# Kernel tuning notes

Hardware: AMD Instinct MI355X
Metric: run time of the kernel (lower is better)

The kernel has to match this reference:

```python
import jax, jax.numpy as jnp
import numpy as np

jax.config.update("jax_enable_x64", True)  # original module runs the filter in float64

SR = 24000
N_CHANNELS = 64
F_MIN, F_MAX = 10.0, 100.0
R_MIN, R_MAX = 0.9999, 0.99999
BATCH, T = 8, 24000


def _make_coeffs():
    # Mirrors BidirectionalCursedIIR.__init__ buffer construction
    freqs = np.exp(np.linspace(np.log(F_MIN), np.log(F_MAX), N_CHANNELS))
    radii = np.linspace(R_MIN, R_MAX, N_CHANNELS)
    theta = 2.0 * np.pi * freqs / SR
    a0 = np.ones_like(radii)
    a1 = -2.0 * radii * np.cos(theta)
    a2 = radii ** 2
    b0 = (1.0 - radii) * 0.5
    a = np.stack([a0, a1, a2], axis=1)                      # [C, 3]
    b = np.stack([b0, np.zeros_like(b0), np.zeros_like(b0)], axis=1)  # [C, 3]
    return jnp.asarray(a, jnp.float64), jnp.asarray(b, jnp.float64)


def _iir_bank(x2d, a1, a2, b0):
    # x2d: [B, T] float64; per-channel recurrence y[n] = b0*x[n] - a1*y[n-1] - a2*y[n-2]
    B = x2d.shape[0]
    C = a1.shape[0]
    z = jnp.zeros((B, C), x2d.dtype)

    def step(carry, xt):  # xt: [B]
        y1, y2 = carry
        y = b0[None, :] * xt[:, None] - a1[None, :] * y1 - a2[None, :] * y2
        return (y, y1), y

    _, ys = jax.lax.scan(step, (z, z), jnp.moveaxis(x2d, 1, 0))  # ys: [T, B, C]
    return jnp.transpose(ys, (1, 2, 0))  # [B, C, T]


def setup_inputs() -> dict:
    key = jax.random.key(0)
    x = jax.random.normal(key, (BATCH, 1, T), dtype=jnp.float32)
    a_coeffs, b_coeffs = _make_coeffs()
    return {"x": x, "a_coeffs": a_coeffs, "b_coeffs": b_coeffs}


def reference(x, a_coeffs, b_coeffs):
    # a0 == 1 by construction, so the normalization by a0 is a no-op
    a1, a2 = a_coeffs[:, 1], a_coeffs[:, 2]
    b0 = b_coeffs[:, 0]
    xd = x[:, 0, :].astype(jnp.float64)  # [B, T]
    fwd_state = _iir_bank(xd, a1, a2, b0)                 # forward pass
    bwd_state = _iir_bank(xd[:, ::-1], a1, a2, b0)[:, :, ::-1]  # flipped pass
    return jnp.concatenate([fwd_state, bwd_state], axis=1).astype(jnp.float32)  # [B, 2C, T]
```

## Files before the change

kernel.cpp:

```cpp
#include <hip/hip_runtime.h>
#include <math.h>

#define T_LEN 24000
#define NCH   64
#define NSEQ  16
#define LCH   192
#define KCH   125
#define KGRP  25

static_assert(KCH * LCH == T_LEN, "chunking must cover T");
static_assert(KCH % KGRP == 0, "grouping must cover KCH");

#define CF_DBL   448
#define ST_DBL   ((size_t)NSEQ * NCH * KCH * 2)
#define WS_FAST  ((CF_DBL + 2 * ST_DBL) * sizeof(double))
#define WS_MID   ((CF_DBL + ST_DBL) * sizeof(double))

__global__ __launch_bounds__(64) void iir_coeffs(double* __restrict__ cf) {
    const int c = threadIdx.x;
    const double l10 = log(10.0), l100 = log(100.0);
    double lf = (c == 63) ? l100 : l10 + (double)c * ((l100 - l10) / 63.0);
    double f  = exp(lf);
    double r  = (c == 63) ? 0.99999
                          : 0.9999 + (double)c * ((0.99999 - 0.9999) / 63.0);
    double th = (2.0 * M_PI) * f / 24000.0;
    double a1 = (-2.0 * r) * cos(th), a2 = r * r, b0 = (1.0 - r) * 0.5;
    double pj1 = 1.0, pj2 = 0.0, pj3 = 0.0;
    #pragma unroll 16
    for (int j = 0; j < LCH; ++j) {
        double p = fma(-a1, pj1, -a2 * pj2);
        pj3 = pj2; pj2 = pj1; pj1 = p;
    }
    cf[0 * 64 + c] = a1;
    cf[1 * 64 + c] = a2;
    cf[2 * 64 + c] = b0;
    cf[3 * 64 + c] = pj1;
    cf[4 * 64 + c] = -a2 * pj2;
    cf[5 * 64 + c] = pj2;
    cf[6 * 64 + c] = -a2 * pj3;
}

__global__ __launch_bounds__(64) void iir_phase1(
        const float* __restrict__ x, const double* __restrict__ cf,
        double* __restrict__ stEnd) {
    __shared__ float xs[LCH];
    const int g = blockIdx.x, k = g % KCH, s = g / KCH;
    const int bi = s >> 1, dir = s & 1, c = threadIdx.x;
    const double a1 = cf[c], a2 = cf[64 + c], b0 = cf[128 + c];
    const float* xb = x + (size_t)bi * T_LEN;
    const int t0 = k * LCH;
    #pragma unroll
    for (int w = 0; w < LCH / 64; ++w) {
        const int t = t0 + w * 64 + c;
        xs[w * 64 + c] = (dir == 0) ? xb[t] : xb[T_LEN - 1 - t];
    }
    __syncthreads();
    double y1 = 0.0, y2 = 0.0;
    #pragma unroll 16
    for (int j = 0; j < LCH; ++j) {
        double y = fma(-a1, y1, fma(-a2, y2, b0 * (double)xs[j]));
        y2 = y1; y1 = y;
    }
    ((double2*)stEnd)[((size_t)k * NSEQ + s) * NCH + c] = make_double2(y1, y2);
}

__global__ __launch_bounds__(64) void iir_phase2(
        const double* __restrict__ cf, const double* __restrict__ stEnd,
        double* __restrict__ stEntry) {
    __shared__ double2 ls[KGRP * NCH];
    const int s = blockIdx.x, c = threadIdx.x;
    const double A00 = cf[192 + c], A01 = cf[256 + c];
    const double A10 = cf[320 + c], A11 = cf[384 + c];
    const double2* src = (const double2*)stEnd;
    double2* dst = (double2*)stEntry;
    double in1 = 0.0, in2 = 0.0;
    for (int g = 0; g < KCH / KGRP; ++g) {
        const int kb = g * KGRP;
        #pragma unroll
        for (int j = 0; j < KGRP; ++j)
            ls[j * NCH + c] = src[((size_t)(kb + j) * NSEQ + s) * NCH + c];
        __syncthreads();
        #pragma unroll
        for (int j = 0; j < KGRP; ++j) {
            const double2 e = ls[j * NCH + c];
            dst[((size_t)(kb + j) * NSEQ + s) * NCH + c] =
                make_double2(in1, in2);
            const double n1 = e.x + fma(A00, in1, A01 * in2);
            const double n2 = e.y + fma(A10, in1, A11 * in2);
            in1 = n1; in2 = n2;
        }
        __syncthreads();
    }
}

__global__ __launch_bounds__(64) void iir_phase2_inplace(
        const double* __restrict__ cf, double* st) {
    __shared__ double2 ls[KGRP * NCH];
    const int s = blockIdx.x, c = threadIdx.x;
    const double A00 = cf[192 + c], A01 = cf[256 + c];
    const double A10 = cf[320 + c], A11 = cf[384 + c];
    double2* buf = (double2*)st;
    double in1 = 0.0, in2 = 0.0;
    for (int g = 0; g < KCH / KGRP; ++g) {
        const int kb = g * KGRP;
        for (int j = 0; j < KGRP; ++j)
            ls[j * NCH + c] = buf[((size_t)(kb + j) * NSEQ + s) * NCH + c];
        __syncthreads();
        for (int j = 0; j < KGRP; ++j) {
            const double2 e = ls[j * NCH + c];
            buf[((size_t)(kb + j) * NSEQ + s) * NCH + c] =
                make_double2(in1, in2);
            const double n1 = e.x + fma(A00, in1, A01 * in2);
            const double n2 = e.y + fma(A10, in1, A11 * in2);
            in1 = n1; in2 = n2;
        }
        __syncthreads();
    }
}

__global__ __launch_bounds__(64) void iir_phase3(
        const float* __restrict__ x, const double* __restrict__ cf,
        const double* __restrict__ stEntry, float* __restrict__ out) {
    __shared__ float xs[LCH];
    __shared__ float tile[NCH][65];
    const int g = blockIdx.x, k = g % KCH, s = g / KCH;
    const int bi = s >> 1, dir = s & 1, c = threadIdx.x;
    const double a1 = cf[c], a2 = cf[64 + c], b0 = cf[128 + c];
    const double2 ent = ((const double2*)stEntry)[((size_t)k * NSEQ + s) * NCH + c];
    double y1 = ent.x, y2 = ent.y;
    const float* xb = x + (size_t)bi * T_LEN;
    const int t0 = k * LCH;
    #pragma unroll
    for (int w = 0; w < LCH / 64; ++w) {
        const int t = t0 + w * 64 + c;
        xs[w * 64 + c] = (dir == 0) ? xb[t] : xb[T_LEN - 1 - t];
    }
    __syncthreads();
    for (int w = 0; w < LCH / 64; ++w) {
        #pragma unroll 16
        for (int jw = 0; jw < 64; ++jw) {
            double y = fma(-a1, y1, fma(-a2, y2, b0 * (double)xs[w * 64 + jw]));
            y2 = y1; y1 = y;
            tile[c][jw] = (float)y;
        }
        __syncthreads();
        const int tw0 = t0 + w * 64;
        if (dir == 0) {
            #pragma unroll
            for (int r = 0; r < NCH; ++r)
                out[((size_t)(bi * 128 + r)) * T_LEN + (tw0 + c)] = tile[r][c];
        } else {
            #pragma unroll
            for (int r = 0; r < NCH; ++r)
                out[((size_t)(bi * 128 + 64 + r)) * T_LEN +
                    (T_LEN - 1 - (tw0 + c))] = tile[r][c];
        }
        __syncthreads();
    }
}

__device__ __forceinline__ void channel_coeffs_dev(int c, double& a1,
                                                   double& a2, double& b0) {
    const double l10 = log(10.0), l100 = log(100.0);
    double lf = (c == 63) ? l100 : l10 + (double)c * ((l100 - l10) / 63.0);
    double f = exp(lf);
    double r = (c == 63) ? 0.99999
                         : 0.9999 + (double)c * ((0.99999 - 0.9999) / 63.0);
    double th = (2.0 * M_PI) * f / 24000.0;
    a1 = (-2.0 * r) * cos(th); a2 = r * r; b0 = (1.0 - r) * 0.5;
}

__global__ __launch_bounds__(64) void iir_direct(
        const float* __restrict__ x, float* __restrict__ out) {
    __shared__ float tile[NCH][65];
    const int s = blockIdx.x, bi = s >> 1, dir = s & 1, c = threadIdx.x;
    double a1, a2, b0;
    channel_coeffs_dev(c, a1, a2, b0);
    const float* xb = x + (size_t)bi * T_LEN;
    double y1 = 0.0, y2 = 0.0;
    for (int t0 = 0; t0 < T_LEN; t0 += 64) {
        #pragma unroll 8
        for (int j = 0; j < 64; ++j) {
            const int t = t0 + j;
            double xv = (dir == 0) ? (double)xb[t] : (double)xb[T_LEN - 1 - t];
            double y = fma(-a1, y1, fma(-a2, y2, b0 * xv));
            y2 = y1; y1 = y;
            tile[c][j] = (float)y;
        }
        __syncthreads();
        if (dir == 0) {
            #pragma unroll
            for (int r = 0; r < NCH; ++r)
                out[((size_t)(bi * 128 + r)) * T_LEN + (t0 + c)] = tile[r][c];
        } else {
            #pragma unroll
            for (int r = 0; r < NCH; ++r)
                out[((size_t)(bi * 128 + 64 + r)) * T_LEN +
                    (T_LEN - 1 - (t0 + c))] = tile[r][c];
        }
        __syncthreads();
    }
}

extern "C" void kernel_launch(void* const* d_in, const int* in_sizes, int n_in,
                              void* d_out, int out_size, void* d_ws, size_t ws_size,
                              hipStream_t stream) {
    const float* x = (const float*)d_in[0];
    float* out = (float*)d_out;
    double* ws = (double*)d_ws;

    if (d_ws != nullptr && ws_size >= WS_FAST) {
        double* cf = ws;
        double* stEnd = ws + CF_DBL;
        double* stEntry = ws + CF_DBL + ST_DBL;
        iir_coeffs<<<1, 64, 0, stream>>>(cf);
        iir_phase1<<<NSEQ * KCH, 64, 0, stream>>>(x, cf, stEnd);
        iir_phase2<<<NSEQ, 64, 0, stream>>>(cf, stEnd, stEntry);
        iir_phase3<<<NSEQ * KCH, 64, 0, stream>>>(x, cf, stEntry, out);
    } else if (d_ws != nullptr && ws_size >= WS_MID) {
        double* cf = ws;
        double* st = ws + CF_DBL;
        iir_coeffs<<<1, 64, 0, stream>>>(cf);
        iir_phase1<<<NSEQ * KCH, 64, 0, stream>>>(x, cf, st);
        iir_phase2_inplace<<<NSEQ, 64, 0, stream>>>(cf, st);
        iir_phase3<<<NSEQ * KCH, 64, 0, stream>>>(x, cf, st, out);
    } else {
        iir_direct<<<NSEQ, 64, 0, stream>>>(x, out);
    }
}
```

Measured before the change: 42.30 us.

## Fold coefficient and carry-propagation kernels into endstate and output kernels

Replaces the four-launch pipeline (coeffs, phase1, serial phase2 scan, phase3) with two launches. Each endstate block computes its channel coefficients inline, and block 0 also writes the chunk-transition matrix. Each output block then redoes the cross-chunk carry scan itself by reading all preceding chunk end states, so the serial 16-block phase2 kernel and the extra launches go away. The cost is redundant O(k) dependent loads and FMAs per block, up to 124 steps for the last chunks, which lengthens the critical path of late blocks.

```diff
diff --git a/kernel.cpp b/kernel.cpp
--- a/kernel.cpp
+++ b/kernel.cpp
@@ -6,47 +6,34 @@
 #define NSEQ  16
 #define LCH   192
 #define KCH   125
-#define KGRP  25
 
 static_assert(KCH * LCH == T_LEN, "chunking must cover T");
-static_assert(KCH % KGRP == 0, "grouping must cover KCH");
 
 #define CF_DBL   448
 #define ST_DBL   ((size_t)NSEQ * NCH * KCH * 2)
-#define WS_FAST  ((CF_DBL + 2 * ST_DBL) * sizeof(double))
-#define WS_MID   ((CF_DBL + ST_DBL) * sizeof(double))
+#define WS_NEED  ((CF_DBL + ST_DBL) * sizeof(double))
 
-__global__ __launch_bounds__(64) void iir_coeffs(double* __restrict__ cf) {
-    const int c = threadIdx.x;
+__device__ __forceinline__ void channel_coeffs_dev(int c, double& a1,
+                                                   double& a2, double& b0) {
     const double l10 = log(10.0), l100 = log(100.0);
     double lf = (c == 63) ? l100 : l10 + (double)c * ((l100 - l10) / 63.0);
     double f  = exp(lf);
     double r  = (c == 63) ? 0.99999
                           : 0.9999 + (double)c * ((0.99999 - 0.9999) / 63.0);
     double th = (2.0 * M_PI) * f / 24000.0;
-    double a1 = (-2.0 * r) * cos(th), a2 = r * r, b0 = (1.0 - r) * 0.5;
-    double pj1 = 1.0, pj2 = 0.0, pj3 = 0.0;
-    #pragma unroll 16
-    for (int j = 0; j < LCH; ++j) {
-        double p = fma(-a1, pj1, -a2 * pj2);
-        pj3 = pj2; pj2 = pj1; pj1 = p;
-    }
-    cf[0 * 64 + c] = a1;
-    cf[1 * 64 + c] = a2;
-    cf[2 * 64 + c] = b0;
-    cf[3 * 64 + c] = pj1;
-    cf[4 * 64 + c] = -a2 * pj2;
-    cf[5 * 64 + c] = pj2;
-    cf[6 * 64 + c] = -a2 * pj3;
+    a1 = (-2.0 * r) * cos(th);
+    a2 = r * r;
+    b0 = (1.0 - r) * 0.5;
 }
 
-__global__ __launch_bounds__(64) void iir_phase1(
-        const float* __restrict__ x, const double* __restrict__ cf,
+__global__ __launch_bounds__(64) void iir_endstates(
+        const float* __restrict__ x, double* __restrict__ cf,
         double* __restrict__ stEnd) {
     __shared__ float xs[LCH];
     const int g = blockIdx.x, k = g % KCH, s = g / KCH;
     const int bi = s >> 1, dir = s & 1, c = threadIdx.x;
-    const double a1 = cf[c], a2 = cf[64 + c], b0 = cf[128 + c];
+    double a1, a2, b0;
+    channel_coeffs_dev(c, a1, a2, b0);
     const float* xb = x + (size_t)bi * T_LEN;
     const int t0 = k * LCH;
     #pragma unroll
@@ -62,72 +49,34 @@
         y2 = y1; y1 = y;
     }
     ((double2*)stEnd)[((size_t)k * NSEQ + s) * NCH + c] = make_double2(y1, y2);
-}
 
-__global__ __launch_bounds__(64) void iir_phase2(
-        const double* __restrict__ cf, const double* __restrict__ stEnd,
-        double* __restrict__ stEntry) {
-    __shared__ double2 ls[KGRP * NCH];
-    const int s = blockIdx.x, c = threadIdx.x;
-    const double A00 = cf[192 + c], A01 = cf[256 + c];
-    const double A10 = cf[320 + c], A11 = cf[384 + c];
-    const double2* src = (const double2*)stEnd;
-    double2* dst = (double2*)stEntry;
-    double in1 = 0.0, in2 = 0.0;
-    for (int g = 0; g < KCH / KGRP; ++g) {
-        const int kb = g * KGRP;
-        #pragma unroll
-        for (int j = 0; j < KGRP; ++j)
-            ls[j * NCH + c] = src[((size_t)(kb + j) * NSEQ + s) * NCH + c];
-        __syncthreads();
-        #pragma unroll
-        for (int j = 0; j < KGRP; ++j) {
-            const double2 e = ls[j * NCH + c];
-            dst[((size_t)(kb + j) * NSEQ + s) * NCH + c] =
-                make_double2(in1, in2);
-            const double n1 = e.x + fma(A00, in1, A01 * in2);
-            const double n2 = e.y + fma(A10, in1, A11 * in2);
-            in1 = n1; in2 = n2;
+    if (g == 0) {
+        double pj1 = 1.0, pj2 = 0.0, pj3 = 0.0;
+        #pragma unroll 16
+        for (int j = 0; j < LCH; ++j) {
+            double p = fma(-a1, pj1, -a2 * pj2);
+            pj3 = pj2; pj2 = pj1; pj1 = p;
         }
-        __syncthreads();
+        cf[0 * 64 + c] = a1;
+        cf[1 * 64 + c] = a2;
+        cf[2 * 64 + c] = b0;
+        cf[3 * 64 + c] = pj1;
+        cf[4 * 64 + c] = -a2 * pj2;
+        cf[5 * 64 + c] = pj2;
+        cf[6 * 64 + c] = -a2 * pj3;
     }
 }
 
-__global__ __launch_bounds__(64) void iir_phase2_inplace(
-        const double* __restrict__ cf, double* st) {
-    __shared__ double2 ls[KGRP * NCH];
-    const int s = blockIdx.x, c = threadIdx.x;
-    const double A00 = cf[192 + c], A01 = cf[256 + c];
-    const double A10 = cf[320 + c], A11 = cf[384 + c];
-    double2* buf = (double2*)st;
-    double in1 = 0.0, in2 = 0.0;
-    for (int g = 0; g < KCH / KGRP; ++g) {
-        const int kb = g * KGRP;
-        for (int j = 0; j < KGRP; ++j)
-            ls[j * NCH + c] = buf[((size_t)(kb + j) * NSEQ + s) * NCH + c];
-        __syncthreads();
-        for (int j = 0; j < KGRP; ++j) {
-            const double2 e = ls[j * NCH + c];
-            buf[((size_t)(kb + j) * NSEQ + s) * NCH + c] =
-                make_double2(in1, in2);
-            const double n1 = e.x + fma(A00, in1, A01 * in2);
-            const double n2 = e.y + fma(A10, in1, A11 * in2);
-            in1 = n1; in2 = n2;
-        }
-        __syncthreads();
-    }
-}
-
-__global__ __launch_bounds__(64) void iir_phase3(
+__global__ __launch_bounds__(64) void iir_output(
         const float* __restrict__ x, const double* __restrict__ cf,
-        const double* __restrict__ stEntry, float* __restrict__ out) {
+        const double* __restrict__ stEnd, float* __restrict__ out) {
     __shared__ float xs[LCH];
     __shared__ float tile[NCH][65];
     const int g = blockIdx.x, k = g % KCH, s = g / KCH;
     const int bi = s >> 1, dir = s & 1, c = threadIdx.x;
-    const double a1 = cf[c], a2 = cf[64 + c], b0 = cf[128 + c];
-    const double2 ent = ((const double2*)stEntry)[((size_t)k * NSEQ + s) * NCH + c];
-    double y1 = ent.x, y2 = ent.y;
+    const double a1  = cf[c],       a2  = cf[64 + c],  b0 = cf[128 + c];
+    const double A00 = cf[192 + c], A01 = cf[256 + c];
+    const double A10 = cf[320 + c], A11 = cf[384 + c];
     const float* xb = x + (size_t)bi * T_LEN;
     const int t0 = k * LCH;
     #pragma unroll
@@ -135,7 +84,17 @@
         const int t = t0 + w * 64 + c;
         xs[w * 64 + c] = (dir == 0) ? xb[t] : xb[T_LEN - 1 - t];
     }
+    const double2* __restrict__ src = (const double2*)stEnd;
+    double in1 = 0.0, in2 = 0.0;
+    #pragma unroll 4
+    for (int j = 0; j < k; ++j) {
+        const double2 e = src[((size_t)j * NSEQ + s) * NCH + c];
+        const double n1 = e.x + fma(A00, in1, A01 * in2);
+        const double n2 = e.y + fma(A10, in1, A11 * in2);
+        in1 = n1; in2 = n2;
+    }
     __syncthreads();
+    double y1 = in1, y2 = in2;
     for (int w = 0; w < LCH / 64; ++w) {
         #pragma unroll 16
         for (int jw = 0; jw < 64; ++jw) {
@@ -157,17 +116,6 @@
         }
         __syncthreads();
     }
-}
-
-__device__ __forceinline__ void channel_coeffs_dev(int c, double& a1,
-                                                   double& a2, double& b0) {
-    const double l10 = log(10.0), l100 = log(100.0);
-    double lf = (c == 63) ? l100 : l10 + (double)c * ((l100 - l10) / 63.0);
-    double f = exp(lf);
-    double r = (c == 63) ? 0.99999
-                         : 0.9999 + (double)c * ((0.99999 - 0.9999) / 63.0);
-    double th = (2.0 * M_PI) * f / 24000.0;
-    a1 = (-2.0 * r) * cos(th); a2 = r * r; b0 = (1.0 - r) * 0.5;
 }
 
 __global__ __launch_bounds__(64) void iir_direct(
@@ -207,23 +155,12 @@
                               hipStream_t stream) {
     const float* x = (const float*)d_in[0];
     float* out = (float*)d_out;
-    double* ws = (double*)d_ws;
 
-    if (d_ws != nullptr && ws_size >= WS_FAST) {
-        double* cf = ws;
-        double* stEnd = ws + CF_DBL;
-        double* stEntry = ws + CF_DBL + ST_DBL;
-        iir_coeffs<<<1, 64, 0, stream>>>(cf);
-        iir_phase1<<<NSEQ * KCH, 64, 0, stream>>>(x, cf, stEnd);
-        iir_phase2<<<NSEQ, 64, 0, stream>>>(cf, stEnd, stEntry);
-        iir_phase3<<<NSEQ * KCH, 64, 0, stream>>>(x, cf, stEntry, out);
-    } else if (d_ws != nullptr && ws_size >= WS_MID) {
-        double* cf = ws;
-        double* st = ws + CF_DBL;
-        iir_coeffs<<<1, 64, 0, stream>>>(cf);
-        iir_phase1<<<NSEQ * KCH, 64, 0, stream>>>(x, cf, st);
-        iir_phase2_inplace<<<NSEQ, 64, 0, stream>>>(cf, st);
-        iir_phase3<<<NSEQ * KCH, 64, 0, stream>>>(x, cf, st, out);
+    if (d_ws != nullptr && ws_size >= WS_NEED) {
+        double* cf = (double*)d_ws;
+        double* stEnd = (double*)d_ws + CF_DBL;
+        iir_endstates<<<NSEQ * KCH, 64, 0, stream>>>(x, cf, stEnd);
+        iir_output<<<NSEQ * KCH, 64, 0, stream>>>(x, cf, stEnd, out);
     } else {
         iir_direct<<<NSEQ, 64, 0, stream>>>(x, out);
     }
```

Result: faster. 38.23 us (-9.6%).
